# Kernel optimization log

Measured on AMD Instinct MI355X. Metric: run time of the kernel, lower is better.

## Reference

```python
import jax, jax.numpy as jnp
import numpy as np

ALPHA = 0.999
BETA = 8
GAMMA = 1
THRESHOLD = 0.5
BATCH, IN_DIM, N_RULES = 8192, 4096, 2048


def setup_inputs() -> dict:
    key = jax.random.key(0)
    kx, kw = jax.random.split(key)
    # x: fuzzy binary features in [0, 1]
    x = jax.random.uniform(kx, (BATCH, IN_DIM), dtype=jnp.float32)
    # W: learned weights, init uniform in [INIT_L=0, 0.5] as in the torch module
    W = 0.5 * jax.random.uniform(kw, (IN_DIM, N_RULES), dtype=jnp.float32)
    return {"x": x, "W": W}


def reference(x, W):
    # Module forward returns the binarized path's VALUE (GradGraft forwards X=res_bar).
    # binarized_forward: Wb = 1[W - 0.5 > 0]; res = (1 - x) @ Wb; out = 1[res <= 0]
    Wb = (W > THRESHOLD).astype(x.dtype)          # [IN_DIM, N_RULES]
    res = (1.0 - x) @ Wb                          # [BATCH, N_RULES]
    return jnp.where(res > 0, jnp.zeros((), x.dtype), jnp.ones((), x.dtype))
```

## Files before the change

kernel.cpp:

```cpp
#include <hip/hip_runtime.h>
#include <stdint.h>

#define BATCH   8192
#define IN_DIM  4096
#define N_RULES 2048
#define NW      (IN_DIM / 64)


__global__ __launch_bounds__(256) void pack_w_kernel(const float* __restrict__ W,
                                                     uint64_t* __restrict__ wt,
                                                     unsigned int* __restrict__ flag) {
    int t    = threadIdx.x;
    int lane = t & 63;
    int wid  = blockIdx.x * 4 + (t >> 6);
    int w     = wid >> 5;
    int jbase = (wid & 31) << 6;
    int j     = jbase + lane;

    const float* Wp = W + (size_t)(w * 64) * N_RULES + j;
    uint64_t word = 0;
#pragma unroll 8
    for (int k = 0; k < 64; ++k) {
        float v = Wp[(size_t)k * N_RULES];
        word |= (uint64_t)(v > 0.5f) << k;
    }
    wt[(size_t)w * N_RULES + j] = word;
    if (word) atomicOr(flag, 1u);
}

__global__ __launch_bounds__(256) void pack_x_kernel(const float* __restrict__ x,
                                                     uint64_t* __restrict__ xb,
                                                     const unsigned int* __restrict__ flag) {
    if (*flag == 0) return;
    int t    = threadIdx.x;
    int lane = t & 63;
    int b    = blockIdx.x * 4 + (t >> 6);
    const float*  xp = x  + (size_t)b * IN_DIM;
    uint64_t*     xo = xb + (size_t)b * NW;
    for (int iter = 0; iter < 16; ++iter) {
        int base = iter * 256;
        uint64_t m0 = __ballot(xp[base +   0 + lane] < 1.0f);
        uint64_t m1 = __ballot(xp[base +  64 + lane] < 1.0f);
        uint64_t m2 = __ballot(xp[base + 128 + lane] < 1.0f);
        uint64_t m3 = __ballot(xp[base + 192 + lane] < 1.0f);
        if (lane == 0) {
            xo[iter * 4 + 0] = m0;  xo[iter * 4 + 1] = m1;
            xo[iter * 4 + 2] = m2;  xo[iter * 4 + 3] = m3;
        }
    }
}

#define BT 128
#define JT 64

__global__ __launch_bounds__(256) void conj_main(const uint64_t* __restrict__ xb,
                                                 const uint64_t* __restrict__ wt,
                                                 float* __restrict__ out) {
    __shared__ uint64_t wlds[JT][65];
    __shared__ int sAny;

    int t  = threadIdx.x;
    int bt = blockIdx.x & 63;
    int jt = blockIdx.x >> 6;
    int bbase = bt * BT;
    int jbase = jt * JT;

    if (t == 0) sAny = 0;
    uint64_t myor = 0;
#pragma unroll
    for (int k = 0; k < 16; ++k) {
        int idx = k * 256 + t;
        int jl = idx & 63, w = idx >> 6;
        uint64_t v = wt[(size_t)w * N_RULES + jbase + jl];
        wlds[jl][w] = v;
        myor |= v;
    }
    __syncthreads();
    if (myor) sAny = 1;
    __syncthreads();

    float4* o4 = (float4*)out;
    const int ldo4 = N_RULES / 4;

    if (sAny == 0) {
        float4 ones = make_float4(1.f, 1.f, 1.f, 1.f);
#pragma unroll
        for (int k = 0; k < 8; ++k) {
            int idx = k * 256 + t;
            int bl = idx >> 4, j4 = idx & 15;
            o4[(size_t)(bbase + bl) * ldo4 + (jbase >> 2) + j4] = ones;
        }
        return;
    }

    int tj = (t & 15) * 4;
    int tb = (t >> 4) * 8;
    unsigned int acc = 0;
    for (int w = 0; w < 64; ++w) {
        uint64_t wj0 = wlds[tj + 0][w];
        uint64_t wj1 = wlds[tj + 1][w];
        uint64_t wj2 = wlds[tj + 2][w];
        uint64_t wj3 = wlds[tj + 3][w];
#pragma unroll
        for (int ib = 0; ib < 8; ++ib) {
            uint64_t xw = xb[(size_t)(bbase + tb + ib) * NW + w];
            unsigned int s = (unsigned)((xw & wj0) != 0)
                           | ((unsigned)((xw & wj1) != 0) << 1)
                           | ((unsigned)((xw & wj2) != 0) << 2)
                           | ((unsigned)((xw & wj3) != 0) << 3);
            acc |= s << (ib * 4);
        }
    }
#pragma unroll
    for (int ib = 0; ib < 8; ++ib) {
        float4 v;
        v.x = ((acc >> (ib * 4 + 0)) & 1) ? 0.f : 1.f;
        v.y = ((acc >> (ib * 4 + 1)) & 1) ? 0.f : 1.f;
        v.z = ((acc >> (ib * 4 + 2)) & 1) ? 0.f : 1.f;
        v.w = ((acc >> (ib * 4 + 3)) & 1) ? 0.f : 1.f;
        o4[(size_t)(bbase + tb + ib) * ldo4 + (jbase >> 2) + (t & 15)] = v;
    }
}

extern "C" void kernel_launch(void* const* d_in, const int* in_sizes, int n_in,
                              void* d_out, int out_size, void* d_ws, size_t ws_size,
                              hipStream_t stream) {
    const float* x = (const float*)d_in[0];
    const float* W = (const float*)d_in[1];
    float* out = (float*)d_out;

    unsigned char* ws   = (unsigned char*)d_ws;
    unsigned int*  flag = (unsigned int*)ws;
    uint64_t*      xb   = (uint64_t*)(ws + 256);
    uint64_t*      wt   = (uint64_t*)(ws + 256 + (size_t)BATCH * NW * sizeof(uint64_t));

    hipMemsetAsync(flag, 0, sizeof(unsigned int), stream);
    pack_w_kernel<<<512, 256, 0, stream>>>(W, wt, flag);
    pack_x_kernel<<<2048, 256, 0, stream>>>(x, xb, flag);
    conj_main<<<64 * 32, 256, 0, stream>>>(xb, wt, out);
}
```

Baseline: 212.0 us.

## Fuse x bit-packing into main kernel and replace atomic flag with per-wave flags

Removes the separate x-packing kernel and memset, packing x tiles into shared memory via ballots inside the main kernel. The global atomic 'any nonzero weight' flag becomes per-wave partial flags, which each block reduces for its column tile to decide the all-ones fast path. This saves a launch and a memset, but in the non-trivial path x is re-packed redundantly by every column-tile block, with extra barriers per word.

Measured after the change: 202.0 us. 1.05x faster.

```diff
diff --git a/kernel.cpp b/kernel.cpp
--- a/kernel.cpp
+++ b/kernel.cpp
@@ -7,9 +7,10 @@
 #define NW      (IN_DIM / 64)
 
 
+
 __global__ __launch_bounds__(256) void pack_w_kernel(const float* __restrict__ W,
                                                      uint64_t* __restrict__ wt,
-                                                     unsigned int* __restrict__ flag) {
+                                                     unsigned int* __restrict__ any_partial) {
     int t    = threadIdx.x;
     int lane = t & 63;
     int wid  = blockIdx.x * 4 + (t >> 6);
@@ -25,39 +26,19 @@
         word |= (uint64_t)(v > 0.5f) << k;
     }
     wt[(size_t)w * N_RULES + j] = word;
-    if (word) atomicOr(flag, 1u);
-}
-
-__global__ __launch_bounds__(256) void pack_x_kernel(const float* __restrict__ x,
-                                                     uint64_t* __restrict__ xb,
-                                                     const unsigned int* __restrict__ flag) {
-    if (*flag == 0) return;
-    int t    = threadIdx.x;
-    int lane = t & 63;
-    int b    = blockIdx.x * 4 + (t >> 6);
-    const float*  xp = x  + (size_t)b * IN_DIM;
-    uint64_t*     xo = xb + (size_t)b * NW;
-    for (int iter = 0; iter < 16; ++iter) {
-        int base = iter * 256;
-        uint64_t m0 = __ballot(xp[base +   0 + lane] < 1.0f);
-        uint64_t m1 = __ballot(xp[base +  64 + lane] < 1.0f);
-        uint64_t m2 = __ballot(xp[base + 128 + lane] < 1.0f);
-        uint64_t m3 = __ballot(xp[base + 192 + lane] < 1.0f);
-        if (lane == 0) {
-            xo[iter * 4 + 0] = m0;  xo[iter * 4 + 1] = m1;
-            xo[iter * 4 + 2] = m2;  xo[iter * 4 + 3] = m3;
-        }
-    }
+    uint64_t nzmask = __ballot(word != 0);
+    if (lane == 0) any_partial[wid] = (nzmask != 0) ? 1u : 0u;
 }
 
 #define BT 128
 #define JT 64
 
-__global__ __launch_bounds__(256) void conj_main(const uint64_t* __restrict__ xb,
+__global__ __launch_bounds__(256) void conj_main(const float* __restrict__ x,
                                                  const uint64_t* __restrict__ wt,
+                                                 const unsigned int* __restrict__ any_partial,
                                                  float* __restrict__ out) {
     __shared__ uint64_t wlds[JT][65];
-    __shared__ int sAny;
+    __shared__ uint64_t xw[BT];
 
     int t  = threadIdx.x;
     int bt = blockIdx.x & 63;
@@ -65,24 +46,13 @@
     int bbase = bt * BT;
     int jbase = jt * JT;
 
-    if (t == 0) sAny = 0;
-    uint64_t myor = 0;
-#pragma unroll
-    for (int k = 0; k < 16; ++k) {
-        int idx = k * 256 + t;
-        int jl = idx & 63, w = idx >> 6;
-        uint64_t v = wt[(size_t)w * N_RULES + jbase + jl];
-        wlds[jl][w] = v;
-        myor |= v;
-    }
-    __syncthreads();
-    if (myor) sAny = 1;
-    __syncthreads();
-
     float4* o4 = (float4*)out;
     const int ldo4 = N_RULES / 4;
 
-    if (sAny == 0) {
+    unsigned int av = any_partial[(t & 63) * 32 + jt];
+    uint64_t nz = __ballot(av != 0);
+
+    if (nz == 0) {
         float4 ones = make_float4(1.f, 1.f, 1.f, 1.f);
 #pragma unroll
         for (int k = 0; k < 8; ++k) {
@@ -93,24 +63,42 @@
         return;
     }
 
+#pragma unroll
+    for (int k = 0; k < 16; ++k) {
+        int idx = k * 256 + t;
+        int jl = idx & 63, w = idx >> 6;
+        wlds[jl][w] = wt[(size_t)w * N_RULES + jbase + jl];
+    }
+
     int tj = (t & 15) * 4;
     int tb = (t >> 4) * 8;
+    int wv   = t >> 6;
+    int lane = t & 63;
     unsigned int acc = 0;
+
     for (int w = 0; w < 64; ++w) {
+        __syncthreads();
+        for (int r = wv; r < BT; r += 4) {
+            uint64_t m = __ballot(x[(size_t)(bbase + r) * IN_DIM + w * 64 + lane] < 1.0f);
+            if (lane == 0) xw[r] = m;
+        }
+        __syncthreads();
+
         uint64_t wj0 = wlds[tj + 0][w];
         uint64_t wj1 = wlds[tj + 1][w];
         uint64_t wj2 = wlds[tj + 2][w];
         uint64_t wj3 = wlds[tj + 3][w];
 #pragma unroll
         for (int ib = 0; ib < 8; ++ib) {
-            uint64_t xw = xb[(size_t)(bbase + tb + ib) * NW + w];
-            unsigned int s = (unsigned)((xw & wj0) != 0)
-                           | ((unsigned)((xw & wj1) != 0) << 1)
-                           | ((unsigned)((xw & wj2) != 0) << 2)
-                           | ((unsigned)((xw & wj3) != 0) << 3);
+            uint64_t xv = xw[tb + ib];
+            unsigned int s = (unsigned)((xv & wj0) != 0)
+                           | ((unsigned)((xv & wj1) != 0) << 1)
+                           | ((unsigned)((xv & wj2) != 0) << 2)
+                           | ((unsigned)((xv & wj3) != 0) << 3);
             acc |= s << (ib * 4);
         }
     }
+
 #pragma unroll
     for (int ib = 0; ib < 8; ++ib) {
         float4 v;
@@ -129,13 +117,10 @@
     const float* W = (const float*)d_in[1];
     float* out = (float*)d_out;
 
-    unsigned char* ws   = (unsigned char*)d_ws;
-    unsigned int*  flag = (unsigned int*)ws;
-    uint64_t*      xb   = (uint64_t*)(ws + 256);
-    uint64_t*      wt   = (uint64_t*)(ws + 256 + (size_t)BATCH * NW * sizeof(uint64_t));
+    unsigned char* ws  = (unsigned char*)d_ws;
+    uint64_t*      wt  = (uint64_t*)ws;
+    unsigned int*  anyp = (unsigned int*)(ws + (size_t)NW * N_RULES * sizeof(uint64_t));
 
-    hipMemsetAsync(flag, 0, sizeof(unsigned int), stream);
-    pack_w_kernel<<<512, 256, 0, stream>>>(W, wt, flag);
-    pack_x_kernel<<<2048, 256, 0, stream>>>(x, xb, flag);
-    conj_main<<<64 * 32, 256, 0, stream>>>(xb, wt, out);
+    pack_w_kernel<<<512, 256, 0, stream>>>(W, wt, anyp);
+    conj_main<<<64 * 32, 256, 0, stream>>>(x, wt, anyp, out);
 }
```
